# Kernel tuning notes

Measured on AMD Instinct MI355X. Metric: run time of the kernel, lower is better.

The kernel has to match this reference:

```python
import jax, jax.numpy as jnp
import numpy as np

K = 9
EPS = 1e-8
TAU2D = 2.0
BASE = jnp.array([[-1, -1], [0, -1], [1, -1], [-1, 0], [0, 0], [1, 0], [-1, 1], [0, 1], [1, 1]], dtype=jnp.float32)


def setup_inputs() -> dict:
    key = jax.random.key(0)
    ks = jax.random.split(key, 8)
    B, C, H, W, N = 4, 64, 256, 256, 16384
    hid, out_dim = 64, 1 + 1 + 2 * K + K
    feat_map = jax.random.normal(ks[0], (B, C, H, W), dtype=jnp.float32)
    coords_2d = jax.random.uniform(ks[1], (B, N, 2), dtype=jnp.float32) * 2.0 - 1.0  # normalized [-1,1]
    cell_2d = jax.random.uniform(ks[2], (B, N, 2), dtype=jnp.float32) * 0.02
    W1 = jax.random.normal(ks[3], (C + 4, hid), dtype=jnp.float32) * 0.05
    b1 = jnp.zeros((hid,), dtype=jnp.float32)
    Wr = jax.random.normal(ks[4], (hid, hid), dtype=jnp.float32) * 0.05
    br = jnp.zeros((hid,), dtype=jnp.float32)
    W2 = jax.random.normal(ks[5], (hid, out_dim), dtype=jnp.float32) * 0.05
    b2 = jnp.zeros((out_dim,), dtype=jnp.float32)
    return {"feat_map": feat_map, "coords_2d": coords_2d, "cell_2d": cell_2d,
            "W1": W1, "b1": b1, "Wr": Wr, "br": br, "W2": W2, "b2": b2}


def _grid_sample_1(feat, grid):
    # feat: (C,H,W), grid: (P,2) normalized coords, bilinear, border pad, align_corners=True
    C, H, W = feat.shape
    ix = jnp.clip((grid[:, 0] + 1.0) * 0.5 * (W - 1), 0.0, W - 1)
    iy = jnp.clip((grid[:, 1] + 1.0) * 0.5 * (H - 1), 0.0, H - 1)
    x0 = jnp.floor(ix)
    y0 = jnp.floor(iy)
    wx = ix - x0
    wy = iy - y0
    x0i = x0.astype(jnp.int32)
    y0i = y0.astype(jnp.int32)
    x1i = jnp.minimum(x0i + 1, W - 1)
    y1i = jnp.minimum(y0i + 1, H - 1)
    f00 = feat[:, y0i, x0i]  # (C,P)
    f01 = feat[:, y0i, x1i]
    f10 = feat[:, y1i, x0i]
    f11 = feat[:, y1i, x1i]
    return (f00 * (1 - wx) * (1 - wy) + f01 * wx * (1 - wy)
            + f10 * (1 - wx) * wy + f11 * wx * wy)  # (C,P)


_grid_sample = jax.vmap(_grid_sample_1)  # (B,C,H,W),(B,P,2)->(B,C,P)


def _leaky(x):
    return jnp.where(x >= 0, x, 0.2 * x)


def _forward(feat_map, coords_2d, cell_2d, W1, b1, Wr, br, W2, b2):
    B, C, H, W = feat_map.shape
    N = coords_2d.shape[1]
    # anchor features
    f_anchor = _grid_sample(feat_map, coords_2d).transpose(0, 2, 1)  # (B,N,C)
    router_in = jnp.concatenate([f_anchor, coords_2d, cell_2d], axis=-1)  # (B,N,C+4)
    h = _leaky(router_in @ W1 + b1)
    h = _leaky(h + (h @ Wr + br))  # residual block
    out = h @ W2 + b2  # (B,N,29)
    r_raw = out[..., 0:1]
    sigma_raw = out[..., 1:2]
    res_raw = out[..., 2:2 + 2 * K]
    gate_raw = out[..., 2 + 2 * K:2 + 3 * K]
    r = jnp.clip(jax.nn.softplus(r_raw) + 0.1, 0.1, 4.0)  # (B,N,1)
    sigma = jnp.clip(jax.nn.softplus(sigma_raw) + 0.5, 0.5, 6.0)  # (B,N,1)
    res = jnp.tanh(res_raw).reshape(B, N, K, 2) * 0.5
    offsets_pix = r[:, :, :, None] * BASE[None, None] + res  # (B,N,K,2)
    scale = jnp.array([2.0 / max(W - 1, 1), 2.0 / max(H - 1, 1)], dtype=jnp.float32)
    offsets_norm = offsets_pix * scale
    deform = coords_2d[:, :, None, :] + offsets_norm  # (B,N,K,2)
    f = _grid_sample(feat_map, deform.reshape(B, N * K, 2))  # (B,C,N*K)
    f = f.reshape(B, C, N, K).transpose(0, 2, 3, 1)  # (B,N,K,C)
    d2 = offsets_pix[..., 0] ** 2 + offsets_pix[..., 1] ** 2  # (B,N,K)
    sig_eff = sigma * TAU2D  # (B,N,1)
    w_geo = jnp.exp(-0.5 * d2 / (sig_eff ** 2 + EPS))
    gate = jax.nn.sigmoid(gate_raw)
    w = w_geo * gate
    w = w / (jnp.sum(w, axis=-1, keepdims=True) + EPS)
    out_feat = jnp.einsum('bnkc,bnk->bnc', f, w)
    return out_feat


def reference(feat_map, coords_2d, cell_2d, W1, b1, Wr, br, W2, b2):
    return _forward(feat_map, coords_2d, cell_2d, W1, b1, Wr, br, W2, b2)
```

## Files before the change

### kernel.cpp

```cpp
#include <hip/hip_runtime.h>

#define K_TAPS 9
#define CC 64
#define HH 256
#define WW 256
#define BB 4
#define NN 16384
#define NPTS (BB * NN)
#define SCLX (2.0f / 255.0f)
#define SCLY (2.0f / 255.0f)
#define AS 68

__device__ __forceinline__ float softplus_f(float x) {
    return fmaxf(x, 0.0f) + log1pf(expf(-fabsf(x)));
}
__device__ __forceinline__ float leaky_f(float x) { return x >= 0.0f ? x : 0.2f * x; }
__device__ __forceinline__ float clampf(float x, float lo, float hi) {
    return fminf(fmaxf(x, lo), hi);
}
__device__ __forceinline__ float bf2f(unsigned short u) {
    union { unsigned int i; float f; } v;
    v.i = (unsigned int)u << 16;
    return v.f;
}
__device__ __forceinline__ unsigned short f2bf(float f) {
    union { float f; unsigned int i; } v;
    v.f = f;
    unsigned int r = (v.i + 0x7FFFu + ((v.i >> 16) & 1u)) >> 16;
    return (unsigned short)r;
}

__global__ void __launch_bounds__(256) transpose_kernel(const float* __restrict__ feat,
                                                        unsigned int* __restrict__ featB) {
    __shared__ float tile[64][65];
    int b = blockIdx.y;
    int p0 = blockIdx.x * 64;
    int tp = threadIdx.x & 63;
    int tq = threadIdx.x >> 6;
    const float* fb = feat + (size_t)b * CC * HH * WW;
#pragma unroll
    for (int i = 0; i < 16; ++i) {
        int c = tq * 16 + i;
        tile[c][tp] = fb[(size_t)c * (HH * WW) + p0 + tp];
    }
    __syncthreads();
    unsigned int* ob = featB + ((size_t)b * (HH * WW) + p0) * 32;
    int c2 = threadIdx.x & 31;
    int psub = threadIdx.x >> 5;
#pragma unroll
    for (int i = 0; i < 8; ++i) {
        int p = i * 8 + psub;
        unsigned int lo = f2bf(tile[2 * c2][p]);
        unsigned int hi = f2bf(tile[2 * c2 + 1][p]);
        ob[(size_t)p * 32 + c2] = lo | (hi << 16);
    }
}

__device__ __forceinline__ float4 bilin4_bf(const unsigned short* __restrict__ base, float gx,
                                            float gy, int c4) {
    float ix = clampf((gx + 1.0f) * 0.5f * 255.0f, 0.0f, 255.0f);
    float iy = clampf((gy + 1.0f) * 0.5f * 255.0f, 0.0f, 255.0f);
    float x0f = floorf(ix), y0f = floorf(iy);
    float wx = ix - x0f, wy = iy - y0f;
    int x0 = (int)x0f, y0 = (int)y0f;
    int x1 = min(x0 + 1, 255), y1 = min(y0 + 1, 255);
    const ushort4 u00 = *(const ushort4*)(base + (size_t)(((y0 << 8) + x0) * 64) + c4 * 4);
    const ushort4 u01 = *(const ushort4*)(base + (size_t)(((y0 << 8) + x1) * 64) + c4 * 4);
    const ushort4 u10 = *(const ushort4*)(base + (size_t)(((y1 << 8) + x0) * 64) + c4 * 4);
    const ushort4 u11 = *(const ushort4*)(base + (size_t)(((y1 << 8) + x1) * 64) + c4 * 4);
    float w00 = (1.0f - wx) * (1.0f - wy), w01 = wx * (1.0f - wy);
    float w10 = (1.0f - wx) * wy, w11 = wx * wy;
    float4 v;
    v.x = bf2f(u00.x) * w00 + bf2f(u01.x) * w01 + bf2f(u10.x) * w10 + bf2f(u11.x) * w11;
    v.y = bf2f(u00.y) * w00 + bf2f(u01.y) * w01 + bf2f(u10.y) * w10 + bf2f(u11.y) * w11;
    v.z = bf2f(u00.z) * w00 + bf2f(u01.z) * w01 + bf2f(u10.z) * w10 + bf2f(u11.z) * w11;
    v.w = bf2f(u00.w) * w00 + bf2f(u01.w) * w01 + bf2f(u10.w) * w10 + bf2f(u11.w) * w11;
    return v;
}

__global__ void __launch_bounds__(256, 5) fused_kernel(const unsigned short* __restrict__ featB,
                                                       const float* __restrict__ coords,
                                                       const float* __restrict__ cell,
                                                       const float* __restrict__ W1,
                                                       const float* __restrict__ b1,
                                                       const float* __restrict__ Wr,
                                                       const float* __restrict__ br,
                                                       const float* __restrict__ W2,
                                                       const float* __restrict__ b2,
                                                       float4* __restrict__ out4) {
    __shared__ __align__(16) unsigned short act[68 * AS];
    __shared__ __align__(16) float wbuf[68 * 64];
    float4* wbuf4 = (float4*)wbuf;

    const int t = threadIdx.x;
    const int q = t & 15;
    const int pgrp = t >> 4;
    const int blk0 = blockIdx.x * 64;

    {
        const int pt = t & 63;
        const int wvi = t >> 6;
        const int pg = blk0 + pt;
        const int bb2 = pg >> 14;
        const float gx = coords[2 * pg], gy = coords[2 * pg + 1];

        const float4* w1g = (const float4*)W1;
        float4 w1r0 = w1g[t];
        float4 w1r1 = w1g[t + 256];
        float4 w1r2 = w1g[t + 512];
        float4 w1r3 = w1g[t + 768];
        float4 w1x;
        if (t < 64) w1x = w1g[1024 + t];

        float ix = clampf((gx + 1.0f) * 0.5f * 255.0f, 0.0f, 255.0f);
        float iy = clampf((gy + 1.0f) * 0.5f * 255.0f, 0.0f, 255.0f);
        float x0f = floorf(ix), y0f = floorf(iy);
        float wx = ix - x0f, wy = iy - y0f;
        int x0 = (int)x0f, y0 = (int)y0f;
        int x1 = min(x0 + 1, 255), y1 = min(y0 + 1, 255);
        const unsigned short* base = featB + (size_t)bb2 * (HH * WW) * 64;
        size_t i00 = (size_t)(((y0 << 8) + x0) * 64), i01 = (size_t)(((y0 << 8) + x1) * 64);
        size_t i10 = (size_t)(((y1 << 8) + x0) * 64), i11 = (size_t)(((y1 << 8) + x1) * 64);
        ushort4 u00[4], u01[4], u10[4], u11[4];
#pragma unroll
        for (int g = 0; g < 4; ++g) {
            int qq = 4 * g + wvi;
            u00[g] = *(const ushort4*)(base + i00 + qq * 4);
            u01[g] = *(const ushort4*)(base + i01 + qq * 4);
            u10[g] = *(const ushort4*)(base + i10 + qq * 4);
            u11[g] = *(const ushort4*)(base + i11 + qq * 4);
        }

        wbuf4[t] = w1r0;
        wbuf4[t + 256] = w1r1;
        wbuf4[t + 512] = w1r2;
        wbuf4[t + 768] = w1r3;
        if (t < 64) wbuf4[1024 + t] = w1x;

        float w00 = (1.0f - wx) * (1.0f - wy), w01 = wx * (1.0f - wy);
        float w10 = (1.0f - wx) * wy, w11 = wx * wy;
#pragma unroll
        for (int g = 0; g < 4; ++g) {
            int qq = 4 * g + wvi;
            float vx = bf2f(u00[g].x) * w00 + bf2f(u01[g].x) * w01 + bf2f(u10[g].x) * w10 +
                       bf2f(u11[g].x) * w11;
            float vy = bf2f(u00[g].y) * w00 + bf2f(u01[g].y) * w01 + bf2f(u10[g].y) * w10 +
                       bf2f(u11[g].y) * w11;
            float vz = bf2f(u00[g].z) * w00 + bf2f(u01[g].z) * w01 + bf2f(u10[g].z) * w10 +
                       bf2f(u11[g].z) * w11;
            float vw = bf2f(u00[g].w) * w00 + bf2f(u01[g].w) * w01 + bf2f(u10[g].w) * w10 +
                       bf2f(u11[g].w) * w11;
            act[(4 * qq + 0) * AS + pt] = f2bf(vx);
            act[(4 * qq + 1) * AS + pt] = f2bf(vy);
            act[(4 * qq + 2) * AS + pt] = f2bf(vz);
            act[(4 * qq + 3) * AS + pt] = f2bf(vw);
        }
        if (wvi == 0) {
            act[64 * AS + pt] = f2bf(gx);
            act[65 * AS + pt] = f2bf(gy);
            act[66 * AS + pt] = f2bf(cell[2 * pg]);
            act[67 * AS + pt] = f2bf(cell[2 * pg + 1]);
        }
    }
    __syncthreads();

    const float4* wrg = (const float4*)Wr;
    float4 wrp0 = wrg[t];
    float4 wrp1 = wrg[t + 256];
    float4 wrp2 = wrg[t + 512];
    float4 wrp3 = wrg[t + 768];

    float hres[4][4];
    {
        float acc[4][4];
        float4 b4 = ((const float4*)b1)[q];
        float bj[4] = {b4.x, b4.y, b4.z, b4.w};
#pragma unroll
        for (int j = 0; j < 4; ++j)
#pragma unroll
            for (int p = 0; p < 4; ++p) acc[j][p] = bj[j];
#pragma unroll 4
        for (int i = 0; i < 68; ++i) {
            ushort4 av = *(const ushort4*)&act[i * AS + 4 * pgrp];
            float4 wv4 = *(const float4*)&wbuf[i * 64 + 4 * q];
            float a[4] = {bf2f(av.x), bf2f(av.y), bf2f(av.z), bf2f(av.w)};
            float wj[4] = {wv4.x, wv4.y, wv4.z, wv4.w};
#pragma unroll
            for (int j = 0; j < 4; ++j)
#pragma unroll
                for (int p = 0; p < 4; ++p) acc[j][p] = fmaf(a[p], wj[j], acc[j][p]);
        }
#pragma unroll
        for (int j = 0; j < 4; ++j)
#pragma unroll
            for (int p = 0; p < 4; ++p) hres[j][p] = leaky_f(acc[j][p]);
    }
    __syncthreads();

#pragma unroll
    for (int j = 0; j < 4; ++j) {
        ushort4 hv;
        hv.x = f2bf(hres[j][0]);
        hv.y = f2bf(hres[j][1]);
        hv.z = f2bf(hres[j][2]);
        hv.w = f2bf(hres[j][3]);
        *(ushort4*)&act[(4 * q + j) * AS + 4 * pgrp] = hv;
    }
    wbuf4[t] = wrp0;
    wbuf4[t + 256] = wrp1;
    wbuf4[t + 512] = wrp2;
    wbuf4[t + 768] = wrp3;
    __syncthreads();

    const float4* w2g = (const float4*)W2;
    float4 w2p0, w2p1;
    if (t < 232) {
        w2p0 = w2g[t];
        w2p1 = w2g[t + 232];
    }

    float h2[4][4];
    {
        float4 b4 = ((const float4*)br)[q];
        float bj[4] = {b4.x, b4.y, b4.z, b4.w};
#pragma unroll
        for (int j = 0; j < 4; ++j)
#pragma unroll
            for (int p = 0; p < 4; ++p) h2[j][p] = bj[j];
#pragma unroll 4
        for (int i = 0; i < 64; ++i) {
            ushort4 av = *(const ushort4*)&act[i * AS + 4 * pgrp];
            float4 wv4 = *(const float4*)&wbuf[i * 64 + 4 * q];
            float a[4] = {bf2f(av.x), bf2f(av.y), bf2f(av.z), bf2f(av.w)};
            float wj[4] = {wv4.x, wv4.y, wv4.z, wv4.w};
#pragma unroll
            for (int j = 0; j < 4; ++j)
#pragma unroll
                for (int p = 0; p < 4; ++p) h2[j][p] = fmaf(a[p], wj[j], h2[j][p]);
        }
#pragma unroll
        for (int j = 0; j < 4; ++j)
#pragma unroll
            for (int p = 0; p < 4; ++p) h2[j][p] = leaky_f(hres[j][p] + h2[j][p]);
    }
    __syncthreads();

#pragma unroll
    for (int j = 0; j < 4; ++j) {
        ushort4 hv;
        hv.x = f2bf(h2[j][0]);
        hv.y = f2bf(h2[j][1]);
        hv.z = f2bf(h2[j][2]);
        hv.w = f2bf(h2[j][3]);
        *(ushort4*)&act[(4 * q + j) * AS + 4 * pgrp] = hv;
    }
    if (t < 232) {
        wbuf4[t] = w2p0;
        wbuf4[t + 232] = w2p1;
    }
    __syncthreads();

    float* sot = wbuf + 2048;
    float* prm = wbuf;

    {
        const int j0 = 2 * q, j1 = 2 * q + 1;
        const int jj0 = min(j0, 28), jj1 = min(j1, 28);
        float o0[4], o1[4];
        float bb0 = b2[jj0], bb1 = b2[jj1];
#pragma unroll
        for (int p = 0; p < 4; ++p) {
            o0[p] = bb0;
            o1[p] = bb1;
        }
#pragma unroll 4
        for (int i = 0; i < 64; ++i) {
            ushort4 av = *(const ushort4*)&act[i * AS + 4 * pgrp];
            float a[4] = {bf2f(av.x), bf2f(av.y), bf2f(av.z), bf2f(av.w)};
            float w0 = wbuf[i * 29 + jj0], w1 = wbuf[i * 29 + jj1];
#pragma unroll
            for (int p = 0; p < 4; ++p) {
                o0[p] = fmaf(a[p], w0, o0[p]);
                o1[p] = fmaf(a[p], w1, o1[p]);
            }
        }
#pragma unroll
        for (int p = 0; p < 4; ++p) {
            int pt = 4 * pgrp + p;
            if (j0 < 29) sot[pt * 30 + j0] = o0[p];
            if (j1 < 29) sot[pt * 30 + j1] = o1[p];
        }
    }
    __syncthreads();

    {
        const int pt = t >> 2, sub = t & 3;
        const int pg = blk0 + pt;
        const float* so = sot + pt * 30;
        float gx = coords[2 * pg], gy = coords[2 * pg + 1];
        float r = clampf(softplus_f(so[0]) + 0.1f, 0.1f, 4.0f);
        float sg = clampf(softplus_f(so[1]) + 0.5f, 0.5f, 6.0f);
        float se = sg * 2.0f;
        float inv2 = -0.5f / (se * se + 1e-8f);
        float sx[3], sy[3], wv[3];
        float s = 0.0f;
#pragma unroll
        for (int ii = 0; ii < 3; ++ii) {
            int kr = 4 * ii + sub;
            int k = kr < 9 ? kr : 0;
            float bx = (float)(k % 3 - 1);
            float by = (float)(k / 3 - 1);
            float ox = fmaf(r, bx, tanhf(so[2 + 2 * k]) * 0.5f);
            float oy = fmaf(r, by, tanhf(so[3 + 2 * k]) * 0.5f);
            float d2 = ox * ox + oy * oy;
            float wgeo = expf(d2 * inv2);
            float gate = 1.0f / (1.0f + expf(-so[20 + k]));
            float w = (kr < 9) ? wgeo * gate : 0.0f;
            wv[ii] = w;
            s += w;
            sx[ii] = fmaf(ox, SCLX, gx);
            sy[ii] = fmaf(oy, SCLY, gy);
        }
        s += __shfl_xor(s, 1, 64);
        s += __shfl_xor(s, 2, 64);
        float inv = 1.0f / (s + 1e-8f);
        float* pp = prm + pt * 28;
#pragma unroll
        for (int ii = 0; ii < 3; ++ii) {
            int kr = 4 * ii + sub;
            if (kr < 9) {
                pp[3 * kr + 0] = sx[ii];
                pp[3 * kr + 1] = sy[ii];
                pp[3 * kr + 2] = wv[ii] * inv;
            }
        }
    }
    __syncthreads();

#pragma unroll
    for (int g2 = 0; g2 < 4; ++g2) {
        int task = g2 * 256 + t;
        int c4 = task & 15;
        int pt = task >> 4;
        int pg = blk0 + pt;
        int bb2 = pg >> 14;
        const unsigned short* base = featB + (size_t)bb2 * (HH * WW) * 64;
        const float* pp = prm + pt * 28;
        float4 acc = make_float4(0.0f, 0.0f, 0.0f, 0.0f);
#pragma unroll 3
        for (int k = 0; k < K_TAPS; ++k) {
            float sx = pp[3 * k + 0];
            float sy = pp[3 * k + 1];
            float wk = pp[3 * k + 2];
            float4 v = bilin4_bf(base, sx, sy, c4);
            acc.x = fmaf(v.x, wk, acc.x);
            acc.y = fmaf(v.y, wk, acc.y);
            acc.z = fmaf(v.z, wk, acc.z);
            acc.w = fmaf(v.w, wk, acc.w);
        }
        out4[(size_t)pg * 16 + c4] = acc;
    }
}

__device__ __forceinline__ float bilin_chw(const float* __restrict__ feat, int b, int lane,
                                           float gx, float gy) {
    float ix = clampf((gx + 1.0f) * 0.5f * 255.0f, 0.0f, 255.0f);
    float iy = clampf((gy + 1.0f) * 0.5f * 255.0f, 0.0f, 255.0f);
    float x0f = floorf(ix), y0f = floorf(iy);
    float wx = ix - x0f, wy = iy - y0f;
    int x0 = (int)x0f, y0 = (int)y0f;
    int x1 = min(x0 + 1, 255), y1 = min(y0 + 1, 255);
    const float* base = feat + ((size_t)b * CC + lane) * (HH * WW);
    float f00 = base[(y0 << 8) + x0];
    float f01 = base[(y0 << 8) + x1];
    float f10 = base[(y1 << 8) + x0];
    float f11 = base[(y1 << 8) + x1];
    float omx = 1.0f - wx, omy = 1.0f - wy;
    return (f00 * omx + f01 * wx) * omy + (f10 * omx + f11 * wx) * wy;
}

__global__ void __launch_bounds__(256) fallback_kernel(const float* __restrict__ feat,
                                                       const float* __restrict__ coords,
                                                       const float* __restrict__ cell,
                                                       const float* __restrict__ W1,
                                                       const float* __restrict__ b1,
                                                       const float* __restrict__ Wr,
                                                       const float* __restrict__ br,
                                                       const float* __restrict__ W2,
                                                       const float* __restrict__ b2,
                                                       float* __restrict__ out) {
    int lane = threadIdx.x & 63;
    int wave = threadIdx.x >> 6;
    int pidx = blockIdx.x * 4 + wave;
    if (pidx >= NPTS) return;
    int b = pidx >> 14;
    float gx = coords[(size_t)pidx * 2 + 0];
    float gy = coords[(size_t)pidx * 2 + 1];
    float cx = cell[(size_t)pidx * 2 + 0];
    float cy = cell[(size_t)pidx * 2 + 1];
    float fa = bilin_chw(feat, b, lane, gx, gy);
    float h = b1[lane];
#pragma unroll
    for (int i = 0; i < 64; ++i) {
        float a = __shfl(fa, i, 64);
        h = fmaf(a, W1[i * 64 + lane], h);
    }
    h = fmaf(gx, W1[64 * 64 + lane], h);
    h = fmaf(gy, W1[65 * 64 + lane], h);
    h = fmaf(cx, W1[66 * 64 + lane], h);
    h = fmaf(cy, W1[67 * 64 + lane], h);
    h = leaky_f(h);
    float h2 = br[lane];
#pragma unroll
    for (int i = 0; i < 64; ++i) {
        float a = __shfl(h, i, 64);
        h2 = fmaf(a, Wr[i * 64 + lane], h2);
    }
    h2 = leaky_f(h + h2);
    int j = lane < 29 ? lane : 0;
    float o = b2[j];
#pragma unroll
    for (int i = 0; i < 64; ++i) {
        float a = __shfl(h2, i, 64);
        o = fmaf(a, W2[i * 29 + j], o);
    }
    int kk = lane < K_TAPS ? lane : 0;
    float r_raw = __shfl(o, 0, 64);
    float s_raw = __shfl(o, 1, 64);
    float rx_raw = __shfl(o, 2 + 2 * kk, 64);
    float ry_raw = __shfl(o, 3 + 2 * kk, 64);
    float g_raw = __shfl(o, 20 + kk, 64);
    float r = clampf(softplus_f(r_raw) + 0.1f, 0.1f, 4.0f);
    float sg = clampf(softplus_f(s_raw) + 0.5f, 0.5f, 6.0f);
    float bx = (float)(kk % 3 - 1);
    float by = (float)(kk / 3 - 1);
    float offx = fmaf(r, bx, tanhf(rx_raw) * 0.5f);
    float offy = fmaf(r, by, tanhf(ry_raw) * 0.5f);
    float d2 = offx * offx + offy * offy;
    float se = sg * 2.0f;
    float wgeo = expf(-0.5f * d2 / (se * se + 1e-8f));
    float gate = 1.0f / (1.0f + expf(-g_raw));
    float w = wgeo * gate;
    float wv = (lane < K_TAPS) ? w : 0.0f;
#pragma unroll
    for (int m = 32; m >= 1; m >>= 1) wv += __shfl_xor(wv, m, 64);
    float wn = w / (wv + 1e-8f);
    float acc = 0.0f;
#pragma unroll
    for (int k = 0; k < K_TAPS; ++k) {
        float ox = __shfl(offx, k, 64) * SCLX;
        float oy = __shfl(offy, k, 64) * SCLY;
        float wk2 = __shfl(wn, k, 64);
        float fv = bilin_chw(feat, b, lane, gx + ox, gy + oy);
        acc = fmaf(fv, wk2, acc);
    }
    out[(size_t)pidx * CC + lane] = acc;
}

extern "C" void kernel_launch(void* const* d_in, const int* in_sizes, int n_in,
                              void* d_out, int out_size, void* d_ws, size_t ws_size,
                              hipStream_t stream) {
    const float* feat = (const float*)d_in[0];
    const float* coords = (const float*)d_in[1];
    const float* cell = (const float*)d_in[2];
    const float* W1 = (const float*)d_in[3];
    const float* b1 = (const float*)d_in[4];
    const float* Wr = (const float*)d_in[5];
    const float* br = (const float*)d_in[6];
    const float* W2 = (const float*)d_in[7];
    const float* b2 = (const float*)d_in[8];
    float* out = (float*)d_out;

    const size_t needT = (size_t)BB * HH * WW * CC * sizeof(unsigned short);

    if (ws_size >= needT) {
        unsigned short* featB = (unsigned short*)d_ws;
        dim3 tg((HH * WW) / 64, BB);
        transpose_kernel<<<tg, 256, 0, stream>>>(feat, (unsigned int*)featB);
        fused_kernel<<<NPTS / 64, 256, 0, stream>>>(featB, coords, cell, W1, b1, Wr, br, W2,
                                                    b2, (float4*)out);
    } else {
        fallback_kernel<<<NPTS / 4, 256, 0, stream>>>(feat, coords, cell, W1, b1, Wr, br, W2,
                                                      b2, out);
    }
}
```

Measured before the change: 75.64 us.

## Halve points per block to 32 and restrict MLP stages to half the threads

```diff
diff --git a/kernel.cpp b/kernel.cpp
--- a/kernel.cpp
+++ b/kernel.cpp
@@ -9,7 +9,8 @@
 #define NPTS (BB * NN)
 #define SCLX (2.0f / 255.0f)
 #define SCLY (2.0f / 255.0f)
-#define AS 68
+#define BPTS 32
+#define AS2 36
 
 __device__ __forceinline__ float softplus_f(float x) {
     return fmaxf(x, 0.0f) + log1pf(expf(-fabsf(x)));
@@ -78,7 +79,7 @@
     return v;
 }
 
-__global__ void __launch_bounds__(256, 5) fused_kernel(const unsigned short* __restrict__ featB,
+__global__ void __launch_bounds__(256, 7) fused_kernel(const unsigned short* __restrict__ featB,
                                                        const float* __restrict__ coords,
                                                        const float* __restrict__ cell,
                                                        const float* __restrict__ W1,
@@ -88,18 +89,18 @@
                                                        const float* __restrict__ W2,
                                                        const float* __restrict__ b2,
                                                        float4* __restrict__ out4) {
-    __shared__ __align__(16) unsigned short act[68 * AS];
+    __shared__ __align__(16) unsigned short act[68 * AS2];
     __shared__ __align__(16) float wbuf[68 * 64];
     float4* wbuf4 = (float4*)wbuf;
 
     const int t = threadIdx.x;
     const int q = t & 15;
     const int pgrp = t >> 4;
-    const int blk0 = blockIdx.x * 64;
+    const int blk0 = blockIdx.x * BPTS;
 
     {
-        const int pt = t & 63;
-        const int wvi = t >> 6;
+        const int pt = t & 31;
+        const int g8 = t >> 5;
         const int pg = blk0 + pt;
         const int bb2 = pg >> 14;
         const float gx = coords[2 * pg], gy = coords[2 * pg + 1];
@@ -121,14 +122,14 @@
         const unsigned short* base = featB + (size_t)bb2 * (HH * WW) * 64;
         size_t i00 = (size_t)(((y0 << 8) + x0) * 64), i01 = (size_t)(((y0 << 8) + x1) * 64);
         size_t i10 = (size_t)(((y1 << 8) + x0) * 64), i11 = (size_t)(((y1 << 8) + x1) * 64);
-        ushort4 u00[4], u01[4], u10[4], u11[4];
-#pragma unroll
-        for (int g = 0; g < 4; ++g) {
-            int qq = 4 * g + wvi;
-            u00[g] = *(const ushort4*)(base + i00 + qq * 4);
-            u01[g] = *(const ushort4*)(base + i01 + qq * 4);
-            u10[g] = *(const ushort4*)(base + i10 + qq * 4);
-            u11[g] = *(const ushort4*)(base + i11 + qq * 4);
+        ushort4 u00[2], u01[2], u10[2], u11[2];
+#pragma unroll
+        for (int hi = 0; hi < 2; ++hi) {
+            int qq = 2 * g8 + hi;
+            u00[hi] = *(const ushort4*)(base + i00 + qq * 4);
+            u01[hi] = *(const ushort4*)(base + i01 + qq * 4);
+            u10[hi] = *(const ushort4*)(base + i10 + qq * 4);
+            u11[hi] = *(const ushort4*)(base + i11 + qq * 4);
         }
 
         wbuf4[t] = w1r0;
@@ -140,26 +141,26 @@
         float w00 = (1.0f - wx) * (1.0f - wy), w01 = wx * (1.0f - wy);
         float w10 = (1.0f - wx) * wy, w11 = wx * wy;
 #pragma unroll
-        for (int g = 0; g < 4; ++g) {
-            int qq = 4 * g + wvi;
-            float vx = bf2f(u00[g].x) * w00 + bf2f(u01[g].x) * w01 + bf2f(u10[g].x) * w10 +
-                       bf2f(u11[g].x) * w11;
-            float vy = bf2f(u00[g].y) * w00 + bf2f(u01[g].y) * w01 + bf2f(u10[g].y) * w10 +
-                       bf2f(u11[g].y) * w11;
-            float vz = bf2f(u00[g].z) * w00 + bf2f(u01[g].z) * w01 + bf2f(u10[g].z) * w10 +
-                       bf2f(u11[g].z) * w11;
-            float vw = bf2f(u00[g].w) * w00 + bf2f(u01[g].w) * w01 + bf2f(u10[g].w) * w10 +
-                       bf2f(u11[g].w) * w11;
-            act[(4 * qq + 0) * AS + pt] = f2bf(vx);
-            act[(4 * qq + 1) * AS + pt] = f2bf(vy);
-            act[(4 * qq + 2) * AS + pt] = f2bf(vz);
-            act[(4 * qq + 3) * AS + pt] = f2bf(vw);
-        }
-        if (wvi == 0) {
-            act[64 * AS + pt] = f2bf(gx);
-            act[65 * AS + pt] = f2bf(gy);
-            act[66 * AS + pt] = f2bf(cell[2 * pg]);
-            act[67 * AS + pt] = f2bf(cell[2 * pg + 1]);
+        for (int hi = 0; hi < 2; ++hi) {
+            int qq = 2 * g8 + hi;
+            float vx = bf2f(u00[hi].x) * w00 + bf2f(u01[hi].x) * w01 + bf2f(u10[hi].x) * w10 +
+                       bf2f(u11[hi].x) * w11;
+            float vy = bf2f(u00[hi].y) * w00 + bf2f(u01[hi].y) * w01 + bf2f(u10[hi].y) * w10 +
+                       bf2f(u11[hi].y) * w11;
+            float vz = bf2f(u00[hi].z) * w00 + bf2f(u01[hi].z) * w01 + bf2f(u10[hi].z) * w10 +
+                       bf2f(u11[hi].z) * w11;
+            float vw = bf2f(u00[hi].w) * w00 + bf2f(u01[hi].w) * w01 + bf2f(u10[hi].w) * w10 +
+                       bf2f(u11[hi].w) * w11;
+            act[(4 * qq + 0) * AS2 + pt] = f2bf(vx);
+            act[(4 * qq + 1) * AS2 + pt] = f2bf(vy);
+            act[(4 * qq + 2) * AS2 + pt] = f2bf(vz);
+            act[(4 * qq + 3) * AS2 + pt] = f2bf(vw);
+        }
+        if (g8 == 0) {
+            act[64 * AS2 + pt] = f2bf(gx);
+            act[65 * AS2 + pt] = f2bf(gy);
+            act[66 * AS2 + pt] = f2bf(cell[2 * pg]);
+            act[67 * AS2 + pt] = f2bf(cell[2 * pg + 1]);
         }
     }
     __syncthreads();
@@ -171,7 +172,7 @@
     float4 wrp3 = wrg[t + 768];
 
     float hres[4][4];
-    {
+    if (t < 128) {
         float acc[4][4];
         float4 b4 = ((const float4*)b1)[q];
         float bj[4] = {b4.x, b4.y, b4.z, b4.w};
@@ -181,7 +182,7 @@
             for (int p = 0; p < 4; ++p) acc[j][p] = bj[j];
 #pragma unroll 4
         for (int i = 0; i < 68; ++i) {
-            ushort4 av = *(const ushort4*)&act[i * AS + 4 * pgrp];
+            ushort4 av = *(const ushort4*)&act[i * AS2 + 4 * pgrp];
             float4 wv4 = *(const float4*)&wbuf[i * 64 + 4 * q];
             float a[4] = {bf2f(av.x), bf2f(av.y), bf2f(av.z), bf2f(av.w)};
             float wj[4] = {wv4.x, wv4.y, wv4.z, wv4.w};
@@ -197,14 +198,16 @@
     }
     __syncthreads();
 
-#pragma unroll
-    for (int j = 0; j < 4; ++j) {
-        ushort4 hv;
-        hv.x = f2bf(hres[j][0]);
-        hv.y = f2bf(hres[j][1]);
-        hv.z = f2bf(hres[j][2]);
-        hv.w = f2bf(hres[j][3]);
-        *(ushort4*)&act[(4 * q + j) * AS + 4 * pgrp] = hv;
+    if (t < 128) {
+#pragma unroll
+        for (int j = 0; j < 4; ++j) {
+            ushort4 hv;
+            hv.x = f2bf(hres[j][0]);
+            hv.y = f2bf(hres[j][1]);
+            hv.z = f2bf(hres[j][2]);
+            hv.w = f2bf(hres[j][3]);
+            *(ushort4*)&act[(4 * q + j) * AS2 + 4 * pgrp] = hv;
+        }
     }
     wbuf4[t] = wrp0;
     wbuf4[t + 256] = wrp1;
@@ -220,7 +223,7 @@
     }
 
     float h2[4][4];
-    {
+    if (t < 128) {
         float4 b4 = ((const float4*)br)[q];
         float bj[4] = {b4.x, b4.y, b4.z, b4.w};
 #pragma unroll
@@ -229,7 +232,7 @@
             for (int p = 0; p < 4; ++p) h2[j][p] = bj[j];
 #pragma unroll 4
         for (int i = 0; i < 64; ++i) {
-            ushort4 av = *(const ushort4*)&act[i * AS + 4 * pgrp];
+            ushort4 av = *(const ushort4*)&act[i * AS2 + 4 * pgrp];
             float4 wv4 = *(const float4*)&wbuf[i * 64 + 4 * q];
             float a[4] = {bf2f(av.x), bf2f(av.y), bf2f(av.z), bf2f(av.w)};
             float wj[4] = {wv4.x, wv4.y, wv4.z, wv4.w};
@@ -245,14 +248,16 @@
     }
     __syncthreads();
 
-#pragma unroll
-    for (int j = 0; j < 4; ++j) {
-        ushort4 hv;
-        hv.x = f2bf(h2[j][0]);
-        hv.y = f2bf(h2[j][1]);
-        hv.z = f2bf(h2[j][2]);
-        hv.w = f2bf(h2[j][3]);
-        *(ushort4*)&act[(4 * q + j) * AS + 4 * pgrp] = hv;
+    if (t < 128) {
+#pragma unroll
+        for (int j = 0; j < 4; ++j) {
+            ushort4 hv;
+            hv.x = f2bf(h2[j][0]);
+            hv.y = f2bf(h2[j][1]);
+            hv.z = f2bf(h2[j][2]);
+            hv.w = f2bf(h2[j][3]);
+            *(ushort4*)&act[(4 * q + j) * AS2 + 4 * pgrp] = hv;
+        }
     }
     if (t < 232) {
         wbuf4[t] = w2p0;
@@ -263,7 +268,7 @@
     float* sot = wbuf + 2048;
     float* prm = wbuf;
 
-    {
+    if (t < 128) {
         const int j0 = 2 * q, j1 = 2 * q + 1;
         const int jj0 = min(j0, 28), jj1 = min(j1, 28);
         float o0[4], o1[4];
@@ -275,7 +280,7 @@
         }
 #pragma unroll 4
         for (int i = 0; i < 64; ++i) {
-            ushort4 av = *(const ushort4*)&act[i * AS + 4 * pgrp];
+            ushort4 av = *(const ushort4*)&act[i * AS2 + 4 * pgrp];
             float a[4] = {bf2f(av.x), bf2f(av.y), bf2f(av.z), bf2f(av.w)};
             float w0 = wbuf[i * 29 + jj0], w1 = wbuf[i * 29 + jj1];
 #pragma unroll
@@ -294,7 +299,7 @@
     __syncthreads();
 
     {
-        const int pt = t >> 2, sub = t & 3;
+        const int pt = t >> 3, sub = t & 7;
         const int pg = blk0 + pt;
         const float* so = sot + pt * 30;
         float gx = coords[2 * pg], gy = coords[2 * pg + 1];
@@ -302,11 +307,11 @@
         float sg = clampf(softplus_f(so[1]) + 0.5f, 0.5f, 6.0f);
         float se = sg * 2.0f;
         float inv2 = -0.5f / (se * se + 1e-8f);
-        float sx[3], sy[3], wv[3];
+        float sx[2], sy[2], wv[2];
         float s = 0.0f;
 #pragma unroll
-        for (int ii = 0; ii < 3; ++ii) {
-            int kr = 4 * ii + sub;
+        for (int ii = 0; ii < 2; ++ii) {
+            int kr = 8 * ii + sub;
             int k = kr < 9 ? kr : 0;
             float bx = (float)(k % 3 - 1);
             float by = (float)(k / 3 - 1);
@@ -323,11 +328,12 @@
         }
         s += __shfl_xor(s, 1, 64);
         s += __shfl_xor(s, 2, 64);
+        s += __shfl_xor(s, 4, 64);
         float inv = 1.0f / (s + 1e-8f);
         float* pp = prm + pt * 28;
 #pragma unroll
-        for (int ii = 0; ii < 3; ++ii) {
-            int kr = 4 * ii + sub;
+        for (int ii = 0; ii < 2; ++ii) {
+            int kr = 8 * ii + sub;
             if (kr < 9) {
                 pp[3 * kr + 0] = sx[ii];
                 pp[3 * kr + 1] = sy[ii];
@@ -338,7 +344,7 @@
     __syncthreads();
 
 #pragma unroll
-    for (int g2 = 0; g2 < 4; ++g2) {
+    for (int g2 = 0; g2 < 2; ++g2) {
         int task = g2 * 256 + t;
         int c4 = task & 15;
         int pt = task >> 4;
@@ -477,8 +483,8 @@
         unsigned short* featB = (unsigned short*)d_ws;
         dim3 tg((HH * WW) / 64, BB);
         transpose_kernel<<<tg, 256, 0, stream>>>(feat, (unsigned int*)featB);
-        fused_kernel<<<NPTS / 64, 256, 0, stream>>>(featB, coords, cell, W1, b1, Wr, br, W2,
-                                                    b2, (float4*)out);
+        fused_kernel<<<NPTS / BPTS, 256, 0, stream>>>(featB, coords, cell, W1, b1, Wr, br, W2,
+                                                      b2, (float4*)out);
     } else {
         fallback_kernel<<<NPTS / 4, 256, 0, stream>>>(feat, coords, cell, W1, b1, Wr, br, W2,
                                                       b2, out);
```

New measurement: 79.12 us. 1.05x slower.
